# Optimization experiments

Measured on AMD Instinct MI355X. Metric: run time of the kernel, lower is better.

## Reference

```python
import jax, jax.numpy as jnp
import numpy as np

D_MODEL = 1024
NUM_HEADS = 16
HEAD_DIM = D_MODEL // NUM_HEADS  # 64
ROPE_BASE = 10000.0


def setup_inputs() -> dict:
    key = jax.random.key(0)
    ks = jax.random.split(key, 12)
    B, S, D = 4, 2048, D_MODEL
    scale = 1.0 / np.sqrt(D)
    inp = {
        'query': jax.random.normal(ks[0], (B, S, D), jnp.float32),
        'key': jax.random.normal(ks[1], (B, S, D), jnp.float32),
        'value': jax.random.normal(ks[2], (B, S, D), jnp.float32),
        'Wq': jax.random.normal(ks[3], (D, D), jnp.float32) * scale,
        'bq': jnp.zeros((D,), jnp.float32),
        'Wk': jax.random.normal(ks[4], (D, D), jnp.float32) * scale,
        'bk': jnp.zeros((D,), jnp.float32),
        'Wv': jax.random.normal(ks[5], (D, D), jnp.float32) * scale,
        'bv': jnp.zeros((D,), jnp.float32),
        'Wo': jax.random.normal(ks[6], (D, D), jnp.float32) * scale,
        'bo': jnp.zeros((D,), jnp.float32),
    }
    return inp


def _rope_cos_sin(seq_len, head_dim, dtype):
    inv_freq = 1.0 / (ROPE_BASE ** (jnp.arange(0, head_dim, 2, dtype=jnp.float32) / head_dim))
    t = jnp.arange(seq_len, dtype=jnp.float32)
    freqs = jnp.einsum('i,j->ij', t, inv_freq)          # [S, hd/2]
    emb = jnp.concatenate([freqs, freqs], axis=-1)      # [S, hd]
    return jnp.cos(emb).astype(dtype), jnp.sin(emb).astype(dtype)


def _rotate_half(x):
    x1, x2 = jnp.split(x, 2, axis=-1)
    return jnp.concatenate([-x2, x1], axis=-1)


def reference(query, key, value, Wq, bq, Wk, bk, Wv, bv, Wo, bo):
    B, T, D = query.shape
    H, hd = NUM_HEADS, HEAD_DIM
    # projections -> [B, H, S, hd]
    Q = (query @ Wq + bq).reshape(B, T, H, hd).transpose(0, 2, 1, 3)
    K = (key @ Wk + bk).reshape(B, -1, H, hd).transpose(0, 2, 1, 3)
    V = (value @ Wv + bv).reshape(B, -1, H, hd).transpose(0, 2, 1, 3)
    # RoPE
    cos, sin = _rope_cos_sin(T, hd, Q.dtype)            # [S, hd]
    Q = Q * cos + _rotate_half(Q) * sin
    K = K * cos + _rotate_half(K) * sin
    # attention
    scores = jnp.einsum('bhtd,bhsd->bhts', Q, K) / jnp.sqrt(jnp.asarray(hd, Q.dtype))
    attn = jax.nn.softmax(scores, axis=-1)
    context = jnp.einsum('bhts,bhsd->bhtd', attn, V)
    context = context.transpose(0, 2, 1, 3).reshape(B, T, D)
    return context @ Wo + bo
```

## Files before the change

### kernel.cpp

```cpp
#include <hip/hip_runtime.h>
#include <hip/hip_bf16.h>
#include <cstdint>
#include <cstddef>

typedef __bf16 bf16_t;
typedef __bf16 bf16x8 __attribute__((ext_vector_type(8)));
typedef __bf16 bf16x4v __attribute__((ext_vector_type(4)));
typedef __bf16 bf16x2v __attribute__((ext_vector_type(2)));
typedef float f32x4 __attribute__((ext_vector_type(4)));
typedef uint32_t u32x4 __attribute__((ext_vector_type(4)));

#define DEVI static __device__ __forceinline__

DEVI void gl_lds16(const void* g, void* l) {
    __builtin_amdgcn_global_load_lds((const __attribute__((address_space(1))) void*)g,
                                     (__attribute__((address_space(3))) void*)l, 16, 0, 0);
}

DEVI float fexp2(float x) {
#if __has_builtin(__builtin_amdgcn_exp2f)
    return __builtin_amdgcn_exp2f(x);
#else
    return __expf(x * 0.6931471805599453f);
#endif
}

DEVI uint32_t pkbf16(float a, float b) {
    bf16x2v t;
    t[0] = (bf16_t)a;
    t[1] = (bf16_t)b;
    return __builtin_bit_cast(uint32_t, t);
}

__global__ __launch_bounds__(256) void castk(const float* __restrict__ i0, const float* __restrict__ i1,
                                             const float* __restrict__ i2, bf16_t* __restrict__ o0,
                                             bf16_t* __restrict__ o1, bf16_t* __restrict__ o2) {
    const float* in = blockIdx.y == 0 ? i0 : blockIdx.y == 1 ? i1 : i2;
    bf16_t* out = blockIdx.y == 0 ? o0 : blockIdx.y == 1 ? o1 : o2;
    size_t i = ((size_t)blockIdx.x * 256 + threadIdx.x) * 4;
    float4 v = *(const float4*)(in + i);
    bf16x4v o;
    o[0] = (bf16_t)v.x; o[1] = (bf16_t)v.y; o[2] = (bf16_t)v.z; o[3] = (bf16_t)v.w;
    *(bf16x4v*)(out + i) = o;
}

__global__ __launch_bounds__(256) void wtrans(const float* __restrict__ W0, const float* __restrict__ W1,
                                              const float* __restrict__ W2, const float* __restrict__ W3,
                                              bf16_t* __restrict__ O0, bf16_t* __restrict__ O1,
                                              bf16_t* __restrict__ O2, bf16_t* __restrict__ O3) {
    const float* W; bf16_t* O;
    switch (blockIdx.z) {
        case 0: W = W0; O = O0; break;
        case 1: W = W1; O = O1; break;
        case 2: W = W2; O = O2; break;
        default: W = W3; O = O3; break;
    }
    __shared__ float t[32][33];
    int tx = threadIdx.x & 31, ty = threadIdx.x >> 5;
    int bx = blockIdx.x * 32, by = blockIdx.y * 32;
#pragma unroll
    for (int yy = 0; yy < 4; ++yy)
        t[ty + yy * 8][tx] = W[(size_t)(by + ty + yy * 8) * 1024 + bx + tx];
    __syncthreads();
#pragma unroll
    for (int yy = 0; yy < 4; ++yy)
        O[(size_t)(bx + ty + yy * 8) * 1024 + by + tx] = (bf16_t)t[tx][ty + yy * 8];
}

__global__ __launch_bounds__(256) void rope_tab(float* __restrict__ ctab, float* __restrict__ stab) {
    int idx = blockIdx.x * 256 + threadIdx.x;
    int s = idx >> 5, i = idx & 31;
    float inv = 1.0f / powf(10000.0f, (float)i * (1.0f / 32.0f));
    float f = (float)s * inv;
    ctab[idx] = cosf(f);
    stab[idx] = sinf(f);
}

__global__ __launch_bounds__(256) void gemm_qkv(const bf16_t* __restrict__ Xq, const bf16_t* __restrict__ Xk,
                                                const bf16_t* __restrict__ Xv, const bf16_t* __restrict__ Wqt,
                                                const bf16_t* __restrict__ Wkt, const bf16_t* __restrict__ Wvt,
                                                const float* __restrict__ bqp, const float* __restrict__ bkp,
                                                const float* __restrict__ bvp, bf16_t* __restrict__ Qo,
                                                bf16_t* __restrict__ Ko, bf16_t* __restrict__ Vo,
                                                const float* __restrict__ ctab, const float* __restrict__ stab) {
    constexpr int K = 1024;
    const int z = blockIdx.z;
    const bf16_t* A  = z == 0 ? Xq : z == 1 ? Xk : Xv;
    const bf16_t* Bt = z == 0 ? Wqt : z == 1 ? Wkt : Wvt;
    const float* bias = z == 0 ? bqp : z == 1 ? bkp : bvp;
    bf16_t* O = z == 0 ? Qo : z == 1 ? Ko : Vo;
    const float scale = z == 0 ? 0.18033688011112042f : 1.0f;

    __shared__ alignas(16) bf16_t As[128 * 32];
    __shared__ alignas(16) bf16_t Bs[128 * 32];
    const int tid = threadIdx.x;
    const int w = tid >> 6, lane = tid & 63, c = lane & 15, qd = lane >> 4;
    const int wm = w >> 1, wn = w & 1;
    const int m0 = blockIdx.x * 128, n0 = blockIdx.y * 128;
    f32x4 acc[4][4] = {};
    for (int kt = 0; kt < K / 32; ++kt) {
#pragma unroll
        for (int l = 0; l < 2; ++l) {
            int e = (l * 256 + tid) * 8;
            int row = e >> 5, col = e & 31;
            gl_lds16(A + (size_t)(m0 + row) * K + kt * 32 + col, (char*)As + (size_t)e * 2);
            gl_lds16(Bt + (size_t)(n0 + row) * K + kt * 32 + col, (char*)Bs + (size_t)e * 2);
        }
        __syncthreads();
        bf16x8 af[4], bfr[4];
#pragma unroll
        for (int i = 0; i < 4; ++i) af[i] = *(const bf16x8*)&As[(wm * 64 + i * 16 + c) * 32 + qd * 8];
#pragma unroll
        for (int j = 0; j < 4; ++j) bfr[j] = *(const bf16x8*)&Bs[(wn * 64 + j * 16 + c) * 32 + qd * 8];
#pragma unroll
        for (int i = 0; i < 4; ++i)
#pragma unroll
            for (int j = 0; j < 4; ++j)
                acc[i][j] = __builtin_amdgcn_mfma_f32_16x16x32_bf16(af[i], bfr[j], acc[i][j], 0, 0, 0);
        __syncthreads();
    }
    const int mb = m0 + wm * 64;
    const int nb = n0 + wn * 64;
    const int h = nb >> 6;
    if (z == 2) {
#pragma unroll
        for (int i = 0; i < 4; ++i) {
            int m = mb + i * 16 + qd * 4;
            int b = m >> 11, s = m & 2047;
#pragma unroll
            for (int j = 0; j < 4; ++j) {
                int d = j * 16 + c;
                float bv = bias[nb + d];
                bf16x4v v4;
#pragma unroll
                for (int r = 0; r < 4; ++r) v4[r] = (bf16_t)(acc[i][j][r] + bv);
                *(bf16x4v*)(O + ((size_t)(b * 16 + h) * 64 + d) * 2048 + s) = v4;
            }
        }
    } else {
#pragma unroll
        for (int i = 0; i < 4; ++i)
#pragma unroll
            for (int jh = 0; jh < 2; ++jh) {
                int d1 = jh * 16 + c;
                float b1 = bias[nb + d1];
                float b2 = bias[nb + d1 + 32];
#pragma unroll
                for (int r = 0; r < 4; ++r) {
                    int m = mb + i * 16 + qd * 4 + r;
                    int b = m >> 11, s = m & 2047;
                    float v1 = acc[i][jh][r] + b1;
                    float v2 = acc[i][jh + 2][r] + b2;
                    float ct = ctab[s * 32 + d1];
                    float st = stab[s * 32 + d1];
                    size_t base = ((size_t)(b * 16 + h) * 2048 + s) * 64;
                    O[base + d1]      = (bf16_t)((v1 * ct - v2 * st) * scale);
                    O[base + d1 + 32] = (bf16_t)((v2 * ct + v1 * st) * scale);
                }
            }
    }
}

__global__ __launch_bounds__(256) void gemm_out(const bf16_t* __restrict__ A, const bf16_t* __restrict__ Bt,
                                                const float* __restrict__ bias, float* __restrict__ O) {
    constexpr int K = 1024, N = 1024;
    __shared__ alignas(16) bf16_t As[128 * 32];
    __shared__ alignas(16) bf16_t Bs[128 * 32];
    const int tid = threadIdx.x;
    const int w = tid >> 6, lane = tid & 63, c = lane & 15, qd = lane >> 4;
    const int wm = w >> 1, wn = w & 1;
    const int m0 = blockIdx.x * 128, n0 = blockIdx.y * 128;
    f32x4 acc[4][4] = {};
    for (int kt = 0; kt < K / 32; ++kt) {
#pragma unroll
        for (int l = 0; l < 2; ++l) {
            int e = (l * 256 + tid) * 8;
            int row = e >> 5, col = e & 31;
            gl_lds16(A + (size_t)(m0 + row) * K + kt * 32 + col, (char*)As + (size_t)e * 2);
            gl_lds16(Bt + (size_t)(n0 + row) * K + kt * 32 + col, (char*)Bs + (size_t)e * 2);
        }
        __syncthreads();
        bf16x8 af[4], bfr[4];
#pragma unroll
        for (int i = 0; i < 4; ++i) af[i] = *(const bf16x8*)&As[(wm * 64 + i * 16 + c) * 32 + qd * 8];
#pragma unroll
        for (int j = 0; j < 4; ++j) bfr[j] = *(const bf16x8*)&Bs[(wn * 64 + j * 16 + c) * 32 + qd * 8];
#pragma unroll
        for (int i = 0; i < 4; ++i)
#pragma unroll
            for (int j = 0; j < 4; ++j)
                acc[i][j] = __builtin_amdgcn_mfma_f32_16x16x32_bf16(af[i], bfr[j], acc[i][j], 0, 0, 0);
        __syncthreads();
    }
    const int mb = m0 + wm * 64, nb = n0 + wn * 64;
#pragma unroll
    for (int i = 0; i < 4; ++i)
#pragma unroll
        for (int j = 0; j < 4; ++j) {
            int n = nb + j * 16 + c;
            float bv = bias[n];
#pragma unroll
            for (int r = 0; r < 4; ++r) {
                int m = mb + i * 16 + qd * 4 + r;
                O[(size_t)m * N + n] = acc[i][j][r] + bv;
            }
        }
}

__global__ __launch_bounds__(256) void attn(const bf16_t* __restrict__ Q, const bf16_t* __restrict__ K,
                                            const bf16_t* __restrict__ Vt, bf16_t* __restrict__ ctx) {
    constexpr int S = 2048;
    __shared__ alignas(16) char smem[32768];
    const int tid = threadIdx.x, w = tid >> 6, lane = tid & 63, c = lane & 15, qd = lane >> 4;
    const int bh = blockIdx.x, q0 = blockIdx.y * 128;
    const bf16_t* Qb = Q + (size_t)bh * S * 64 + (size_t)q0 * 64;
    const bf16_t* Kb = K + (size_t)bh * S * 64;
    const bf16_t* Vb = Vt + (size_t)bh * 64 * S;
#pragma unroll
    for (int l = 0; l < 4; ++l) {
        int slot = l * 256 + tid;
        int row = slot >> 3, ch = slot & 7;
        int sch = ch ^ ((row >> 1) & 7);
        gl_lds16(Qb + (size_t)row * 64 + sch * 8, smem + (size_t)slot * 16);
    }
    __syncthreads();
    const int rch = (c >> 1) & 7;
    bf16x8 qf[2][2];
    {
        const bf16_t* Qs = (const bf16_t*)smem;
#pragma unroll
        for (int kk = 0; kk < 2; ++kk) {
            const int ch = (4 * kk + qd) ^ rch;
#pragma unroll
            for (int i = 0; i < 2; ++i)
                qf[kk][i] = *(const bf16x8*)&Qs[(w * 32 + i * 16 + c) * 64 + ch * 8];
        }
    }
    __syncthreads();
    auto stageKV = [&](int kt, int buf) {
        const int s0 = kt * 64;
        char* kbase = smem + buf * 16384;
        char* vbase = kbase + 8192;
#pragma unroll
        for (int l = 0; l < 2; ++l) {
            int slot = l * 256 + tid;
            int row = slot >> 3, ch = slot & 7;
            int sch = ch ^ ((row >> 1) & 7);
            gl_lds16(Kb + (size_t)(s0 + row) * 64 + sch * 8, kbase + (size_t)slot * 16);
            gl_lds16(Vb + (size_t)row * S + s0 + sch * 8, vbase + (size_t)slot * 16);
        }
    };
    stageKV(0, 0);
    __syncthreads();
    const int srcA = c + ((lane >> 4) & 1) * 32;
    const int srcB = srcA + 16;
    const bool hisel = (qd >> 1) & 1;
    f32x4 acc_o[2][4] = {};
    float ls[2] = {0.f, 0.f};
    const f32x4 Z = {0.f, 0.f, 0.f, 0.f};
    for (int kt = 0; kt < S / 64; ++kt) {
        const int cur = kt & 1;
        if (kt + 1 < S / 64) stageKV(kt + 1, cur ^ 1);
        const bf16_t* KsC = (const bf16_t*)(smem + cur * 16384);
        const bf16_t* VsC = (const bf16_t*)(smem + cur * 16384 + 8192);
        f32x4 sc[4][2];
#pragma unroll
        for (int kk = 0; kk < 2; ++kk) {
            const int ch = (4 * kk + qd) ^ rch;
            bf16x8 kf[4];
#pragma unroll
            for (int j = 0; j < 4; ++j) kf[j] = *(const bf16x8*)&KsC[(j * 16 + c) * 64 + ch * 8];
#pragma unroll
            for (int j = 0; j < 4; ++j)
#pragma unroll
                for (int i = 0; i < 2; ++i)
                    sc[j][i] = __builtin_amdgcn_mfma_f32_16x16x32_bf16(kf[j], qf[kk][i],
                                                                       kk == 0 ? Z : sc[j][i], 0, 0, 0);
        }
        uint32_t pku[4][2][2];
#pragma unroll
        for (int j = 0; j < 4; ++j)
#pragma unroll
            for (int i = 0; i < 2; ++i) {
                float p0 = fexp2(sc[j][i][0]), p1 = fexp2(sc[j][i][1]);
                float p2 = fexp2(sc[j][i][2]), p3 = fexp2(sc[j][i][3]);
                ls[i] += (p0 + p1) + (p2 + p3);
                pku[j][i][0] = pkbf16(p0, p1);
                pku[j][i][1] = pkbf16(p2, p3);
            }
#pragma unroll
        for (int kk = 0; kk < 2; ++kk) {
            const int ch = (4 * kk + qd) ^ rch;
            bf16x8 vf[4];
#pragma unroll
            for (int j = 0; j < 4; ++j) vf[j] = *(const bf16x8*)&VsC[(j * 16 + c) * 64 + ch * 8];
#pragma unroll
            for (int i = 0; i < 2; ++i) {
                uint32_t a0, a1, a2, a3;
                {
                    uint32_t lo = __shfl(pku[2 * kk][i][0], srcA);
                    uint32_t hi = __shfl(pku[2 * kk + 1][i][0], srcA);
                    a0 = hisel ? hi : lo;
                    lo = __shfl(pku[2 * kk][i][1], srcA);
                    hi = __shfl(pku[2 * kk + 1][i][1], srcA);
                    a1 = hisel ? hi : lo;
                    lo = __shfl(pku[2 * kk][i][0], srcB);
                    hi = __shfl(pku[2 * kk + 1][i][0], srcB);
                    a2 = hisel ? hi : lo;
                    lo = __shfl(pku[2 * kk][i][1], srcB);
                    hi = __shfl(pku[2 * kk + 1][i][1], srcB);
                    a3 = hisel ? hi : lo;
                }
                u32x4 av = {a0, a1, a2, a3};
                bf16x8 af = __builtin_bit_cast(bf16x8, av);
#pragma unroll
                for (int j = 0; j < 4; ++j)
                    acc_o[i][j] = __builtin_amdgcn_mfma_f32_16x16x32_bf16(af, vf[j], acc_o[i][j], 0, 0, 0);
            }
        }
        __syncthreads();
    }
    float linv[2][4];
#pragma unroll
    for (int i = 0; i < 2; ++i) {
        float v = ls[i];
        v += __shfl_xor(v, 16);
        v += __shfl_xor(v, 32);
        float vinv = 1.0f / v;
#pragma unroll
        for (int r = 0; r < 4; ++r)
            linv[i][r] = __shfl(vinv, qd * 20 + r);
    }
    const int b = bh >> 4, h = bh & 15;
#pragma unroll
    for (int i = 0; i < 2; ++i)
#pragma unroll
        for (int j = 0; j < 4; ++j)
#pragma unroll
            for (int r = 0; r < 4; ++r) {
                int qrow = q0 + w * 32 + i * 16 + qd * 4 + r;
                float o = acc_o[i][j][r] * linv[i][r];
                ctx[((size_t)(b * 2048 + qrow)) * 1024 + (size_t)h * 64 + j * 16 + c] = (bf16_t)o;
            }
}

extern "C" void kernel_launch(void* const* d_in, const int* in_sizes, int n_in,
                              void* d_out, int out_size, void* d_ws, size_t ws_size,
                              hipStream_t stream) {
    (void)in_sizes; (void)n_in; (void)out_size; (void)ws_size;
    const float* query = (const float*)d_in[0];
    const float* key   = (const float*)d_in[1];
    const float* value = (const float*)d_in[2];
    const float* Wq = (const float*)d_in[3];
    const float* bq = (const float*)d_in[4];
    const float* Wk = (const float*)d_in[5];
    const float* bk = (const float*)d_in[6];
    const float* Wv = (const float*)d_in[7];
    const float* bv = (const float*)d_in[8];
    const float* Wo = (const float*)d_in[9];
    const float* bo = (const float*)d_in[10];

    const size_t SZ = (size_t)8192 * 1024;
    bf16_t* Xq = (bf16_t*)d_ws;
    bf16_t* Xk = Xq + SZ;
    bf16_t* Xv = Xk + SZ;
    bf16_t* Qb = Xv + SZ;
    bf16_t* Kb = Qb + SZ;
    bf16_t* Vtb = Kb + SZ;
    bf16_t* Wqt = Vtb + SZ;
    bf16_t* Wkt = Wqt + 1024 * 1024;
    bf16_t* Wvt = Wkt + 1024 * 1024;
    bf16_t* Wot = Wvt + 1024 * 1024;
    float* ctab = (float*)(Wot + 1024 * 1024);
    float* stab = ctab + 2048 * 32;
    bf16_t* CT = Xq;

    castk<<<dim3(8192, 3), 256, 0, stream>>>(query, key, value, Xq, Xk, Xv);
    wtrans<<<dim3(32, 32, 4), 256, 0, stream>>>(Wq, Wk, Wv, Wo, Wqt, Wkt, Wvt, Wot);
    rope_tab<<<256, 256, 0, stream>>>(ctab, stab);
    gemm_qkv<<<dim3(64, 8, 3), 256, 0, stream>>>(Xq, Xk, Xv, Wqt, Wkt, Wvt, bq, bk, bv,
                                                 Qb, Kb, Vtb, ctab, stab);
    attn<<<dim3(64, 16), 256, 0, stream>>>(Qb, Kb, Vtb, CT);
    gemm_out<<<dim3(64, 8), 256, 0, stream>>>(CT, Wot, bo, (float*)d_out);
}
```

Before: 392.1 us.

## Switch attention to 32x32x16 MFMA with 256-query tiles and MFMA row sums

Result: faster. 363.2 us (-7.4%).

```diff
diff --git a/kernel.cpp b/kernel.cpp
--- a/kernel.cpp
+++ b/kernel.cpp
@@ -8,6 +8,7 @@
 typedef __bf16 bf16x4v __attribute__((ext_vector_type(4)));
 typedef __bf16 bf16x2v __attribute__((ext_vector_type(2)));
 typedef float f32x4 __attribute__((ext_vector_type(4)));
+typedef float f32x16 __attribute__((ext_vector_type(16)));
 typedef uint32_t u32x4 __attribute__((ext_vector_type(4)));
 
 #define DEVI static __device__ __forceinline__
@@ -211,30 +212,29 @@
                                             const bf16_t* __restrict__ Vt, bf16_t* __restrict__ ctx) {
     constexpr int S = 2048;
     __shared__ alignas(16) char smem[32768];
-    const int tid = threadIdx.x, w = tid >> 6, lane = tid & 63, c = lane & 15, qd = lane >> 4;
-    const int bh = blockIdx.x, q0 = blockIdx.y * 128;
+    const int tid = threadIdx.x, w = tid >> 6, lane = tid & 63;
+    const int lo5 = lane & 31, hi = lane >> 5;
+    const int rm = (lo5 >> 1) & 7;
+    const int bh = blockIdx.x, q0 = blockIdx.y * 256;
     const bf16_t* Qb = Q + (size_t)bh * S * 64 + (size_t)q0 * 64;
     const bf16_t* Kb = K + (size_t)bh * S * 64;
     const bf16_t* Vb = Vt + (size_t)bh * 64 * S;
 #pragma unroll
-    for (int l = 0; l < 4; ++l) {
+    for (int l = 0; l < 8; ++l) {
         int slot = l * 256 + tid;
         int row = slot >> 3, ch = slot & 7;
         int sch = ch ^ ((row >> 1) & 7);
         gl_lds16(Qb + (size_t)row * 64 + sch * 8, smem + (size_t)slot * 16);
     }
     __syncthreads();
-    const int rch = (c >> 1) & 7;
-    bf16x8 qf[2][2];
+    bf16x8 qf[4][2];
     {
         const bf16_t* Qs = (const bf16_t*)smem;
 #pragma unroll
-        for (int kk = 0; kk < 2; ++kk) {
-            const int ch = (4 * kk + qd) ^ rch;
-#pragma unroll
-            for (int i = 0; i < 2; ++i)
-                qf[kk][i] = *(const bf16x8*)&Qs[(w * 32 + i * 16 + c) * 64 + ch * 8];
-        }
+        for (int kc = 0; kc < 4; ++kc)
+#pragma unroll
+            for (int qb = 0; qb < 2; ++qb)
+                qf[kc][qb] = *(const bf16x8*)&Qs[(size_t)(w * 64 + qb * 32 + lo5) * 64 + ((kc * 2 + hi) ^ rm) * 8];
     }
     __syncthreads();
     auto stageKV = [&](int kt, int buf) {
@@ -251,97 +251,84 @@
         }
     };
     stageKV(0, 0);
+    f32x16 acc_o[2][2] = {};
+    f32x16 acc_l[2] = {};
+    const f32x16 Z16 = {};
+    bf16x8 ones;
+    {
+        u32x4 ov = {0x3F803F80u, 0x3F803F80u, 0x3F803F80u, 0x3F803F80u};
+        ones = __builtin_bit_cast(bf16x8, ov);
+    }
     __syncthreads();
-    const int srcA = c + ((lane >> 4) & 1) * 32;
-    const int srcB = srcA + 16;
-    const bool hisel = (qd >> 1) & 1;
-    f32x4 acc_o[2][4] = {};
-    float ls[2] = {0.f, 0.f};
-    const f32x4 Z = {0.f, 0.f, 0.f, 0.f};
     for (int kt = 0; kt < S / 64; ++kt) {
         const int cur = kt & 1;
         if (kt + 1 < S / 64) stageKV(kt + 1, cur ^ 1);
         const bf16_t* KsC = (const bf16_t*)(smem + cur * 16384);
         const bf16_t* VsC = (const bf16_t*)(smem + cur * 16384 + 8192);
-        f32x4 sc[4][2];
-#pragma unroll
-        for (int kk = 0; kk < 2; ++kk) {
-            const int ch = (4 * kk + qd) ^ rch;
-            bf16x8 kf[4];
-#pragma unroll
-            for (int j = 0; j < 4; ++j) kf[j] = *(const bf16x8*)&KsC[(j * 16 + c) * 64 + ch * 8];
-#pragma unroll
-            for (int j = 0; j < 4; ++j)
-#pragma unroll
-                for (int i = 0; i < 2; ++i)
-                    sc[j][i] = __builtin_amdgcn_mfma_f32_16x16x32_bf16(kf[j], qf[kk][i],
-                                                                       kk == 0 ? Z : sc[j][i], 0, 0, 0);
-        }
-        uint32_t pku[4][2][2];
-#pragma unroll
-        for (int j = 0; j < 4; ++j)
-#pragma unroll
-            for (int i = 0; i < 2; ++i) {
-                float p0 = fexp2(sc[j][i][0]), p1 = fexp2(sc[j][i][1]);
-                float p2 = fexp2(sc[j][i][2]), p3 = fexp2(sc[j][i][3]);
-                ls[i] += (p0 + p1) + (p2 + p3);
-                pku[j][i][0] = pkbf16(p0, p1);
-                pku[j][i][1] = pkbf16(p2, p3);
-            }
-#pragma unroll
-        for (int kk = 0; kk < 2; ++kk) {
-            const int ch = (4 * kk + qd) ^ rch;
-            bf16x8 vf[4];
-#pragma unroll
-            for (int j = 0; j < 4; ++j) vf[j] = *(const bf16x8*)&VsC[(j * 16 + c) * 64 + ch * 8];
-#pragma unroll
-            for (int i = 0; i < 2; ++i) {
-                uint32_t a0, a1, a2, a3;
-                {
-                    uint32_t lo = __shfl(pku[2 * kk][i][0], srcA);
-                    uint32_t hi = __shfl(pku[2 * kk + 1][i][0], srcA);
-                    a0 = hisel ? hi : lo;
-                    lo = __shfl(pku[2 * kk][i][1], srcA);
-                    hi = __shfl(pku[2 * kk + 1][i][1], srcA);
-                    a1 = hisel ? hi : lo;
-                    lo = __shfl(pku[2 * kk][i][0], srcB);
-                    hi = __shfl(pku[2 * kk + 1][i][0], srcB);
-                    a2 = hisel ? hi : lo;
-                    lo = __shfl(pku[2 * kk][i][1], srcB);
-                    hi = __shfl(pku[2 * kk + 1][i][1], srcB);
-                    a3 = hisel ? hi : lo;
-                }
-                u32x4 av = {a0, a1, a2, a3};
+        f32x16 st[2][2];
+#pragma unroll
+        for (int kc = 0; kc < 4; ++kc) {
+            bf16x8 kf[2];
+#pragma unroll
+            for (int sb = 0; sb < 2; ++sb)
+                kf[sb] = *(const bf16x8*)&KsC[(size_t)(sb * 32 + lo5) * 64 + ((kc * 2 + hi) ^ rm) * 8];
+#pragma unroll
+            for (int sb = 0; sb < 2; ++sb)
+#pragma unroll
+                for (int qb = 0; qb < 2; ++qb)
+                    st[sb][qb] = __builtin_amdgcn_mfma_f32_32x32x16_bf16(kf[sb], qf[kc][qb],
+                                                                         kc == 0 ? Z16 : st[sb][qb], 0, 0, 0);
+        }
+        uint32_t pku[2][2][8];
+#pragma unroll
+        for (int sb = 0; sb < 2; ++sb)
+#pragma unroll
+            for (int qb = 0; qb < 2; ++qb)
+#pragma unroll
+                for (int u = 0; u < 8; ++u)
+                    pku[sb][qb][u] = pkbf16(fexp2(st[sb][qb][2 * u]), fexp2(st[sb][qb][2 * u + 1]));
+#pragma unroll
+        for (int skc = 0; skc < 4; ++skc) {
+            bf16x8 vf[2];
+#pragma unroll
+            for (int db = 0; db < 2; ++db)
+                vf[db] = *(const bf16x8*)&VsC[(size_t)(db * 32 + lo5) * 64 + ((skc * 2 + hi) ^ rm) * 8];
+            const int sb = skc >> 1, b = (skc & 1) * 4;
+#pragma unroll
+            for (int qb = 0; qb < 2; ++qb) {
+                uint32_t p0 = pku[sb][qb][b + 0], p1 = pku[sb][qb][b + 1];
+                uint32_t p2 = pku[sb][qb][b + 2], p3 = pku[sb][qb][b + 3];
+                uint32_t send0 = hi ? p0 : p2;
+                uint32_t send1 = hi ? p1 : p3;
+                uint32_t recv0 = __shfl_xor(send0, 32);
+                uint32_t recv1 = __shfl_xor(send1, 32);
+                u32x4 av = {hi ? recv0 : p0, hi ? recv1 : p1,
+                            hi ? p2 : recv0, hi ? p3 : recv1};
                 bf16x8 af = __builtin_bit_cast(bf16x8, av);
-#pragma unroll
-                for (int j = 0; j < 4; ++j)
-                    acc_o[i][j] = __builtin_amdgcn_mfma_f32_16x16x32_bf16(af, vf[j], acc_o[i][j], 0, 0, 0);
-            }
-        }
-        __syncthreads();
-    }
-    float linv[2][4];
-#pragma unroll
-    for (int i = 0; i < 2; ++i) {
-        float v = ls[i];
-        v += __shfl_xor(v, 16);
-        v += __shfl_xor(v, 32);
-        float vinv = 1.0f / v;
-#pragma unroll
-        for (int r = 0; r < 4; ++r)
-            linv[i][r] = __shfl(vinv, qd * 20 + r);
+                acc_l[qb] = __builtin_amdgcn_mfma_f32_32x32x16_bf16(af, ones, acc_l[qb], 0, 0, 0);
+#pragma unroll
+                for (int db = 0; db < 2; ++db)
+                    acc_o[qb][db] = __builtin_amdgcn_mfma_f32_32x32x16_bf16(af, vf[db], acc_o[qb][db], 0, 0, 0);
+            }
+        }
+        __syncthreads();
     }
     const int b = bh >> 4, h = bh & 15;
 #pragma unroll
-    for (int i = 0; i < 2; ++i)
-#pragma unroll
-        for (int j = 0; j < 4; ++j)
-#pragma unroll
-            for (int r = 0; r < 4; ++r) {
-                int qrow = q0 + w * 32 + i * 16 + qd * 4 + r;
-                float o = acc_o[i][j][r] * linv[i][r];
-                ctx[((size_t)(b * 2048 + qrow)) * 1024 + (size_t)h * 64 + j * 16 + c] = (bf16_t)o;
-            }
+    for (int qb = 0; qb < 2; ++qb) {
+        float linv[16];
+#pragma unroll
+        for (int r = 0; r < 16; ++r) linv[r] = 1.0f / acc_l[qb][r];
+#pragma unroll
+        for (int db = 0; db < 2; ++db)
+#pragma unroll
+            for (int r = 0; r < 16; ++r) {
+                int qrow = q0 + w * 64 + qb * 32 + (r & 3) + 8 * (r >> 2) + 4 * hi;
+                int d = db * 32 + lo5;
+                float o = acc_o[qb][db][r] * linv[r];
+                ctx[((size_t)(b * 2048 + qrow)) * 1024 + (size_t)h * 64 + d] = (bf16_t)o;
+            }
+    }
 }
 
 extern "C" void kernel_launch(void* const* d_in, const int* in_sizes, int n_in,
@@ -380,6 +367,6 @@
     rope_tab<<<256, 256, 0, stream>>>(ctab, stab);
     gemm_qkv<<<dim3(64, 8, 3), 256, 0, stream>>>(Xq, Xk, Xv, Wqt, Wkt, Wvt, bq, bk, bv,
                                                  Qb, Kb, Vtb, ctab, stab);
-    attn<<<dim3(64, 16), 256, 0, stream>>>(Qb, Kb, Vtb, CT);
+    attn<<<dim3(64, 8), 256, 0, stream>>>(Qb, Kb, Vtb, CT);
     gemm_out<<<dim3(64, 8), 256, 0, stream>>>(CT, Wot, bo, (float*)d_out);
 }
```
